# Kernel optimization log

Measured on AMD Instinct MI355X. Metric: run time of the kernel, lower is better.

## Reference

```python
import jax, jax.numpy as jnp
import numpy as np

K = 20          # args.k (minu=True)
EPS = 1e-5      # BatchNorm eps
BNS = float(1.0 / np.sqrt(1.0 + EPS))  # eval-mode BN with running_mean=0, running_var=1


def knn_idx(x, k):
    # x: (B, C, N); returns indices of k nearest neighbors (incl. self): (B, N, k)
    xx = jnp.sum(x * x, axis=1)                       # (B, N)
    inner = jnp.einsum('bcn,bcm->bnm', x, x)          # (B, N, N)
    dist = 2.0 * inner - xx[:, :, None] - xx[:, None, :]  # = -||xi - xj||^2
    return jax.lax.top_k(dist, k)[1]


def graph_feature(x, k):
    # x: (B, C, N) -> edge features (B, 2C, N, k) = cat(neighbor - center, center)
    idx = knn_idx(x, k)                               # (B, N, k)
    xt = jnp.transpose(x, (0, 2, 1))                  # (B, N, C)
    feat = jnp.take_along_axis(xt[:, None, :, :], idx[..., None], axis=2)  # (B, N, k, C)
    center = xt[:, :, None, :]
    out = jnp.concatenate([feat - center, jnp.broadcast_to(center, feat.shape)], axis=-1)
    return jnp.transpose(out, (0, 3, 1, 2))


def edge_block(x, w, g, b, k):
    # EdgeConv: gather -> 1x1 conv -> BN(eval) -> LeakyReLU(0.2) -> max over neighbors
    h = graph_feature(x, k)                           # (B, 2C, N, k)
    y = jnp.einsum('bcnk,oc->bonk', h, w)
    y = g[None, :, None, None] * (y * BNS) + b[None, :, None, None]
    y = jax.nn.leaky_relu(y, 0.2)
    return jnp.max(y, axis=-1)                        # (B, O, N)


def _bn1(v, g, b):
    return g * (v * BNS) + b


def setup_inputs() -> dict:
    key = jax.random.key(0)
    ks = jax.random.split(key, 32)
    B, C, N = 16, 6, 1024

    def w(k_, shape):
        return jax.random.normal(k_, shape, jnp.float32) / np.sqrt(shape[1])

    def gm(k_, n):
        return 1.0 + 0.1 * jax.random.normal(k_, (n,), jnp.float32)

    def bt(k_, n):
        return 0.1 * jax.random.normal(k_, (n,), jnp.float32)

    return {
        'x': jax.random.normal(ks[0], (B, C, N), jnp.float32),
        'disc': jax.random.normal(ks[1], (B, 1), jnp.float32),
        'w1': w(ks[2], (64, 12)),   'g1': gm(ks[3], 64),   'b1': bt(ks[4], 64),
        'w2': w(ks[5], (64, 128)),  'g2': gm(ks[6], 64),   'b2': bt(ks[7], 64),
        'w3': w(ks[8], (128, 128)), 'g3': gm(ks[9], 128),  'b3': bt(ks[10], 128),
        'w4': w(ks[11], (256, 256)),'g4': gm(ks[12], 256), 'b4': bt(ks[13], 256),
        'w5': w(ks[14], (1024, 512)),'g5': gm(ks[15], 1024),'b5': bt(ks[16], 1024),
        'wl1': w(ks[17], (256, 2048)),'g6': gm(ks[18], 256),'b6': bt(ks[19], 256),
        'wl2': w(ks[20], (128, 256)),'g7': gm(ks[21], 128),'b7': bt(ks[22], 128),
        'wl21': w(ks[23], (64, 128)),
        'wl22': w(ks[24], (32, 64)),'g8': gm(ks[25], 32), 'b8': bt(ks[26], 32),
        'wl3': w(ks[27], (90, 32)),
    }


def reference(x, disc, w1, g1, b1, w2, g2, b2, w3, g3, b3, w4, g4, b4,
              w5, g5, b5, wl1, g6, b6, wl2, g7, b7, wl21, wl22, g8, b8, wl3):
    # disc is accepted by the original forward but unused
    x1 = edge_block(x, w1, g1, b1, K)                 # (B, 64, N)
    x2 = edge_block(x1, w2, g2, b2, K)                # (B, 64, N)
    x3 = edge_block(x2, w3, g3, b3, K)                # (B, 128, N)
    x4 = edge_block(x3, w4, g4, b4, K)                # (B, 256, N)
    h = jnp.concatenate([x1, x2, x3, x4], axis=1)     # (B, 512, N)
    y = jnp.einsum('bcn,oc->bon', h, w5)              # conv5 1x1
    y = g5[None, :, None] * (y * BNS) + b5[None, :, None]
    y = jax.nn.leaky_relu(y, 0.2)                     # (B, emb, N)
    p = jnp.concatenate([jnp.max(y, axis=2), jnp.mean(y, axis=2)], axis=1)  # (B, 2*emb)
    z = jax.nn.leaky_relu(_bn1(p @ wl1.T, g6, b6), 0.2)
    z = jax.nn.leaky_relu(_bn1(z @ wl2.T, g7, b7), 0.2)
    z = jax.nn.gelu(_bn1((z @ wl21.T) @ wl22.T, g8, b8), approximate=False)
    return z @ wl3.T                                  # (B, 90)
```

## Files before the change

### kernel.cpp

```cpp
#include <hip/hip_runtime.h>
#include <math.h>
#include <float.h>

#define BNS_C 0.9999950000374996f

typedef __bf16 bf8 __attribute__((ext_vector_type(8)));
typedef float f4 __attribute__((ext_vector_type(4)));
union I4BF8 { int4 i; bf8 b; };

static __device__ __forceinline__ unsigned short f2bf(float f) {
    unsigned u = __float_as_uint(f);
    u += 0x7fff + ((u >> 16) & 1);
    return (unsigned short)(u >> 16);
}

__global__ void k_xin_t(const float* __restrict__ x, float* __restrict__ X0, float* __restrict__ xx) {
    int i = blockIdx.x * 256 + threadIdx.x;
    int b = i >> 10, n = i & 1023;
    const float* xb = x + (((size_t)b * 6) << 10) + n;
    float4* o4 = (float4*)(X0 + ((size_t)i << 3));
    float v0 = xb[0], v1 = xb[1 << 10], v2 = xb[2 << 10];
    float v3 = xb[3 << 10], v4 = xb[4 << 10], v5 = xb[5 << 10];
    o4[0] = make_float4(v0, v1, v2, v3);
    o4[1] = make_float4(v4, v5, 0.f, 0.f);
    xx[i] = v0*v0 + v1*v1 + v2*v2 + v3*v3 + v4*v4 + v5*v5;
}

__global__ __launch_bounds__(256) void k_gram2(const float* __restrict__ X, const float* __restrict__ xx,
                                               float* __restrict__ D, int Cp, int b0) {
    int z = blockIdx.z, b = b0 + z;
    int n0 = blockIdx.y * 64, m0 = blockIdx.x * 64;
    __shared__ float As[32 * 68], Bs[32 * 68];
    int tid = threadIdx.x;
    int ti = tid & 15, tj = tid >> 4;
    float acc[4][4] = {};
    const float* Xb = X + (((size_t)b) << 10) * Cp;
    for (int c0 = 0; c0 < Cp; c0 += 32) {
        for (int e = tid; e < 2048; e += 256) {
            int row = e >> 5, cc = e & 31, c = c0 + cc;
            float a = 0.f, bb = 0.f;
            if (c < Cp) {
                a  = Xb[(size_t)(n0 + row) * Cp + c];
                bb = Xb[(size_t)(m0 + row) * Cp + c];
            }
            As[cc * 68 + row] = a; Bs[cc * 68 + row] = bb;
        }
        __syncthreads();
#pragma unroll 8
        for (int cc = 0; cc < 32; ++cc) {
            const float4 av = *(const float4*)(As + cc * 68 + 4 * tj);
            const float4 bv = *(const float4*)(Bs + cc * 68 + 4 * ti);
            acc[0][0] += av.x * bv.x; acc[0][1] += av.x * bv.y; acc[0][2] += av.x * bv.z; acc[0][3] += av.x * bv.w;
            acc[1][0] += av.y * bv.x; acc[1][1] += av.y * bv.y; acc[1][2] += av.y * bv.z; acc[1][3] += av.y * bv.w;
            acc[2][0] += av.z * bv.x; acc[2][1] += av.z * bv.y; acc[2][2] += av.z * bv.z; acc[2][3] += av.z * bv.w;
            acc[3][0] += av.w * bv.x; acc[3][1] += av.w * bv.y; acc[3][2] += av.w * bv.z; acc[3][3] += av.w * bv.w;
        }
        __syncthreads();
    }
    const float4 xm = *(const float4*)(xx + (b << 10) + m0 + 4 * ti);
#pragma unroll
    for (int a = 0; a < 4; ++a) {
        int n = n0 + 4 * tj + a;
        float xn = xx[(b << 10) + n];
        float4 o;
        o.x = 2.f * acc[a][0] - xn - xm.x;
        o.y = 2.f * acc[a][1] - xn - xm.y;
        o.z = 2.f * acc[a][2] - xn - xm.z;
        o.w = 2.f * acc[a][3] - xn - xm.w;
        *(float4*)(D + ((size_t)((z << 10) + n) << 10) + m0 + 4 * ti) = o;
    }
}

#define CE(I,J) { if (kk[I] < kk[J]) { unsigned long long t_ = kk[I]; kk[I] = kk[J]; kk[J] = t_; } }
__global__ __launch_bounds__(256) void k_topk(const float* __restrict__ D, int* __restrict__ idxo, int b0) {
    __shared__ unsigned long long H[4096];
    int lane = threadIdx.x & 63, wv = threadIdx.x >> 6;
    int rl = blockIdx.x * 4 + wv;
    const float* row = D + ((size_t)rl << 10);
    unsigned long long kk[16];
#pragma unroll
    for (int j = 0; j < 16; ++j) {
        float v = row[lane + 64 * j];
        unsigned u = __float_as_uint(v);
        unsigned s = u ^ ((unsigned)(((int)u) >> 31) | 0x80000000u);
        int m = lane + (j << 6);
        kk[j] = ((unsigned long long)s << 32) | (unsigned)(1023 - m);
    }
    CE(0,1) CE(2,3) CE(0,2) CE(1,3) CE(1,2)
    CE(4,5) CE(6,7) CE(4,6) CE(5,7) CE(5,6)
    CE(0,4) CE(2,6) CE(2,4) CE(1,5) CE(3,7) CE(3,5) CE(1,2) CE(3,4) CE(5,6)
    CE(8,9) CE(10,11) CE(8,10) CE(9,11) CE(9,10)
    CE(12,13) CE(14,15) CE(12,14) CE(13,15) CE(13,14)
    CE(8,12) CE(10,14) CE(10,12) CE(9,13) CE(11,15) CE(11,13) CE(9,10) CE(11,12) CE(13,14)
    CE(0,8) CE(4,12) CE(4,8) CE(2,10) CE(6,14) CE(6,10) CE(2,4) CE(6,8) CE(10,12)
    CE(1,9) CE(5,13) CE(5,9) CE(3,11) CE(7,15) CE(7,11) CE(3,5) CE(7,9) CE(11,13)
    CE(1,2) CE(3,4) CE(5,6) CE(7,8) CE(9,10) CE(11,12) CE(13,14)
    unsigned long long* Hw = H + (wv << 10);
#pragma unroll
    for (int j = 0; j < 16; ++j) Hw[(j << 6) + lane] = kk[j];
    int ptr = 0;
    unsigned long long h = kk[0];
    int* outp = idxo + (size_t)((b0 << 10) + rl) * 20;
    for (int it = 0; it < 20; ++it) {
        unsigned long long bk = h;
#pragma unroll
        for (int off = 32; off; off >>= 1) {
            unsigned long long ok = __shfl_down(bk, off);
            if (ok > bk) bk = ok;
        }
        unsigned wlo = __builtin_amdgcn_readfirstlane((unsigned)bk);
        unsigned whi = __builtin_amdgcn_readfirstlane((unsigned)(bk >> 32));
        unsigned long long win = ((unsigned long long)whi << 32) | wlo;
        if (lane == 0) outp[it] = 1023 - (int)(wlo & 1023);
        if (h == win) {
            ++ptr;
            h = (ptr < 16) ? Hw[(ptr << 6) + lane] : 0ULL;
        }
    }
}
#undef CE

__global__ __launch_bounds__(256) void k_uv(const float* __restrict__ X, const float* __restrict__ w,
                                            float* __restrict__ V, float* __restrict__ U,
                                            int Cp, int C, int O) {
    int n0 = blockIdx.x * 64, o0 = blockIdx.y * 64, b = blockIdx.z;
    __shared__ float Xs[32 * 68], Was[32 * 68], Wds[32 * 68];
    int tid = threadIdx.x, ti = tid & 15, tj = tid >> 4;
    float accv[4][4] = {}, accu[4][4] = {};
    const float* Xb = X + (((size_t)b) << 10) * Cp;
    int W2 = 2 * C;
    for (int c0 = 0; c0 < Cp; c0 += 32) {
        for (int e = tid; e < 2048; e += 256) {
            int row = e >> 5, cc = e & 31, c = c0 + cc;
            Xs[cc * 68 + row] = (c < Cp) ? Xb[(size_t)(n0 + row) * Cp + c] : 0.f;
            float wa = 0.f, wd = 0.f;
            if (c < C) {
                float a_ = w[(size_t)(o0 + row) * W2 + c];
                float b_ = w[(size_t)(o0 + row) * W2 + C + c];
                wa = a_; wd = b_ - a_;
            }
            Was[cc * 68 + row] = wa; Wds[cc * 68 + row] = wd;
        }
        __syncthreads();
#pragma unroll 8
        for (int cc = 0; cc < 32; ++cc) {
            const float4 xv = *(const float4*)(Xs  + cc * 68 + 4 * tj);
            const float4 av = *(const float4*)(Was + cc * 68 + 4 * ti);
            const float4 dv = *(const float4*)(Wds + cc * 68 + 4 * ti);
            accv[0][0] += xv.x * av.x; accv[0][1] += xv.x * av.y; accv[0][2] += xv.x * av.z; accv[0][3] += xv.x * av.w;
            accv[1][0] += xv.y * av.x; accv[1][1] += xv.y * av.y; accv[1][2] += xv.y * av.z; accv[1][3] += xv.y * av.w;
            accv[2][0] += xv.z * av.x; accv[2][1] += xv.z * av.y; accv[2][2] += xv.z * av.z; accv[2][3] += xv.z * av.w;
            accv[3][0] += xv.w * av.x; accv[3][1] += xv.w * av.y; accv[3][2] += xv.w * av.z; accv[3][3] += xv.w * av.w;
            accu[0][0] += xv.x * dv.x; accu[0][1] += xv.x * dv.y; accu[0][2] += xv.x * dv.z; accu[0][3] += xv.x * dv.w;
            accu[1][0] += xv.y * dv.x; accu[1][1] += xv.y * dv.y; accu[1][2] += xv.y * dv.z; accu[1][3] += xv.y * dv.w;
            accu[2][0] += xv.z * dv.x; accu[2][1] += xv.z * dv.y; accu[2][2] += xv.z * dv.z; accu[2][3] += xv.z * dv.w;
            accu[3][0] += xv.w * dv.x; accu[3][1] += xv.w * dv.y; accu[3][2] += xv.w * dv.z; accu[3][3] += xv.w * dv.w;
        }
        __syncthreads();
    }
#pragma unroll
    for (int a = 0; a < 4; ++a) {
        int n = n0 + 4 * tj + a;
        size_t base = ((size_t)((b << 10) + n)) * O + o0 + 4 * ti;
        *(float4*)(V + base) = make_float4(accv[a][0], accv[a][1], accv[a][2], accv[a][3]);
        *(float4*)(U + base) = make_float4(accu[a][0], accu[a][1], accu[a][2], accu[a][3]);
    }
}

__global__ __launch_bounds__(256) void k_gmax(const float* __restrict__ V, const float* __restrict__ U,
                                              const int* __restrict__ idx,
                                              const float* __restrict__ gg, const float* __restrict__ bb,
                                              float* __restrict__ Xo, float* __restrict__ xx,
                                              unsigned short* __restrict__ HB, int coff, int O) {
    __shared__ float sxx[4];
    int tid = threadIdx.x;
    int Tn = 256 / O;
    int j = tid / O, o = tid - j * O;
    int pt = blockIdx.x * Tn + j;
    int b = pt >> 10, n = pt & 1023;
    float uv = U[(size_t)pt * O + o];
    float gv = gg[o], bv = bb[o];
    const int* ip = idx + (size_t)pt * 20;
    float mx = -FLT_MAX;
    for (int k = 0; k < 20; ++k) {
        int m = ip[k] & 1023;
        float vv = V[(size_t)((b << 10) + m) * O + o];
        float y = gv * ((vv + uv) * BNS_C) + bv;
        y = y > 0.f ? y : 0.2f * y;
        mx = fmaxf(mx, y);
    }
    Xo[(size_t)pt * O + o] = mx;
    int c = coff + o;
    HB[(((size_t)(b * 16 + (c >> 5)) << 10) + n) * 32 + (c & 31)] = f2bf(mx);
    float s = mx * mx;
#pragma unroll
    for (int off = 32; off; off >>= 1) s += __shfl_down(s, off);
    int wid = tid >> 6, lane = tid & 63;
    if (lane == 0) sxx[wid] = s;
    __syncthreads();
    if (o == 0) {
        int Wpp = O >> 6;
        float t = 0.f;
        for (int w = 0; w < Wpp; ++w) t += sxx[j * Wpp + w];
        xx[pt] = t;
    }
}

__global__ __launch_bounds__(256) void k_final_mfma(const unsigned short* __restrict__ HB,
                                                    const float* __restrict__ w5,
                                                    const float* __restrict__ g5,
                                                    const float* __restrict__ b5,
                                                    float* __restrict__ pp) {
    int b = blockIdx.x;
    int nt = blockIdx.z;
    int wv = threadIdx.x >> 6, lane = threadIdx.x & 63;
    int r = lane & 15, q = lane >> 4;
    int o = blockIdx.y * 64 + wv * 16 + r;
    bf8 Bfr[16];
    const float* wrow = w5 + (size_t)o * 512 + q * 8;
#pragma unroll
    for (int s = 0; s < 16; ++s) {
        float4 f0 = *(const float4*)(wrow + s * 32);
        float4 f1 = *(const float4*)(wrow + s * 32 + 4);
        I4BF8 u_;
        u_.i.x = f2bf(f0.x) | ((unsigned)f2bf(f0.y) << 16);
        u_.i.y = f2bf(f0.z) | ((unsigned)f2bf(f0.w) << 16);
        u_.i.z = f2bf(f1.x) | ((unsigned)f2bf(f1.y) << 16);
        u_.i.w = f2bf(f1.z) | ((unsigned)f2bf(f1.w) << 16);
        Bfr[s] = u_.b;
    }
    float gb = g5[o] * BNS_C, bv = b5[o];
    float mx = -FLT_MAX, sm = 0.f;
    for (int g = 0; g < 4; ++g) {
        int row0 = (nt << 8) + (g << 6);
        f4 C0 = {0.f, 0.f, 0.f, 0.f}, C1 = C0, C2 = C0, C3 = C0;
#pragma unroll
        for (int s = 0; s < 16; ++s) {
            const unsigned short* slab = HB + (((size_t)(b * 16 + s) << 10) + row0) * 32 + q * 8;
            I4BF8 A0, A1, A2, A3;
            A0.i = *(const int4*)(slab + (size_t)( 0 + r) * 32);
            A1.i = *(const int4*)(slab + (size_t)(16 + r) * 32);
            A2.i = *(const int4*)(slab + (size_t)(32 + r) * 32);
            A3.i = *(const int4*)(slab + (size_t)(48 + r) * 32);
            C0 = __builtin_amdgcn_mfma_f32_16x16x32_bf16(A0.b, Bfr[s], C0, 0, 0, 0);
            C1 = __builtin_amdgcn_mfma_f32_16x16x32_bf16(A1.b, Bfr[s], C1, 0, 0, 0);
            C2 = __builtin_amdgcn_mfma_f32_16x16x32_bf16(A2.b, Bfr[s], C2, 0, 0, 0);
            C3 = __builtin_amdgcn_mfma_f32_16x16x32_bf16(A3.b, Bfr[s], C3, 0, 0, 0);
        }
#pragma unroll
        for (int e = 0; e < 4; ++e) {
            float y0 = gb * C0[e] + bv; y0 = y0 > 0.f ? y0 : 0.2f * y0; mx = fmaxf(mx, y0); sm += y0;
            float y1 = gb * C1[e] + bv; y1 = y1 > 0.f ? y1 : 0.2f * y1; mx = fmaxf(mx, y1); sm += y1;
            float y2 = gb * C2[e] + bv; y2 = y2 > 0.f ? y2 : 0.2f * y2; mx = fmaxf(mx, y2); sm += y2;
            float y3 = gb * C3[e] + bv; y3 = y3 > 0.f ? y3 : 0.2f * y3; mx = fmaxf(mx, y3); sm += y3;
        }
    }
    mx = fmaxf(mx, __shfl_down(mx, 32)); sm += __shfl_down(sm, 32);
    mx = fmaxf(mx, __shfl_down(mx, 16)); sm += __shfl_down(sm, 16);
    if (q == 0) {
        float* pb = pp + (size_t)(nt * 16 + b) * 2048;
        pb[o] = mx;
        pb[1024 + o] = sm;
    }
}

__global__ __launch_bounds__(256) void k_fc2p(const float* __restrict__ pp, const float* __restrict__ w,
                                              const float* __restrict__ gg, const float* __restrict__ bb,
                                              float* __restrict__ out, int O) {
    int gw = blockIdx.x * 4 + (threadIdx.x >> 6);
    int lane = threadIdx.x & 63;
    int r = gw / O, o = gw - r * O;
    const float* wr = w + (size_t)o * 2048;
    float s = 0.f;
    for (int c = lane; c < 2048; c += 64) {
        const float* q0 = pp + (size_t)r * 2048 + c;
        float v;
        if (c < 1024) {
            v = fmaxf(fmaxf(q0[0], q0[16 * 2048]), fmaxf(q0[32 * 2048], q0[48 * 2048]));
        } else {
            v = (q0[0] + q0[16 * 2048] + q0[32 * 2048] + q0[48 * 2048]) * (1.f / 1024.f);
        }
        s += v * wr[c];
    }
#pragma unroll
    for (int off = 32; off; off >>= 1) s += __shfl_down(s, off);
    if (lane == 0) {
        float y = gg[o] * (s * BNS_C) + bb[o];
        out[gw] = y > 0.f ? y : 0.2f * y;
    }
}

__global__ __launch_bounds__(256) void k_fc_tail(const float* __restrict__ z1,
                                                 const float* __restrict__ wl2, const float* __restrict__ g7, const float* __restrict__ b7,
                                                 const float* __restrict__ wl21,
                                                 const float* __restrict__ wl22, const float* __restrict__ g8, const float* __restrict__ b8,
                                                 const float* __restrict__ wl3,
                                                 float* __restrict__ out) {
    __shared__ float L1[128], L2[64], L3[32];
    int r = blockIdx.x;
    int tid = threadIdx.x, lane = tid & 63, wv = tid >> 6;
    const float* ir = z1 + r * 256;
    float a0 = ir[lane], a1 = ir[lane + 64], a2 = ir[lane + 128], a3 = ir[lane + 192];
    for (int ob = 0; ob < 32; ob += 2) {
        int o0 = wv * 32 + ob, o1 = o0 + 1;
        const float* w0 = wl2 + (size_t)o0 * 256;
        const float* w1 = wl2 + (size_t)o1 * 256;
        float s0 = a0 * w0[lane] + a1 * w0[lane + 64] + a2 * w0[lane + 128] + a3 * w0[lane + 192];
        float s1 = a0 * w1[lane] + a1 * w1[lane + 64] + a2 * w1[lane + 128] + a3 * w1[lane + 192];
#pragma unroll
        for (int off = 32; off; off >>= 1) { s0 += __shfl_down(s0, off); s1 += __shfl_down(s1, off); }
        if (lane == 0) {
            float y0 = g7[o0] * (s0 * BNS_C) + b7[o0]; L1[o0] = y0 > 0.f ? y0 : 0.2f * y0;
            float y1 = g7[o1] * (s1 * BNS_C) + b7[o1]; L1[o1] = y1 > 0.f ? y1 : 0.2f * y1;
        }
    }
    __syncthreads();
    float b0v = L1[lane], b1v = L1[lane + 64];
    for (int ob = 0; ob < 16; ob += 2) {
        int o0 = wv * 16 + ob, o1 = o0 + 1;
        const float* w0 = wl21 + (size_t)o0 * 128;
        const float* w1 = wl21 + (size_t)o1 * 128;
        float s0 = b0v * w0[lane] + b1v * w0[lane + 64];
        float s1 = b0v * w1[lane] + b1v * w1[lane + 64];
#pragma unroll
        for (int off = 32; off; off >>= 1) { s0 += __shfl_down(s0, off); s1 += __shfl_down(s1, off); }
        if (lane == 0) { L2[o0] = s0; L2[o1] = s1; }
    }
    __syncthreads();
    float c0v = L2[lane];
    for (int ob = 0; ob < 8; ob += 2) {
        int o0 = wv * 8 + ob, o1 = o0 + 1;
        float s0 = c0v * wl22[(size_t)o0 * 64 + lane];
        float s1 = c0v * wl22[(size_t)o1 * 64 + lane];
#pragma unroll
        for (int off = 32; off; off >>= 1) { s0 += __shfl_down(s0, off); s1 += __shfl_down(s1, off); }
        if (lane == 0) {
            float y0 = g8[o0] * (s0 * BNS_C) + b8[o0];
            L3[o0] = 0.5f * y0 * (1.f + erff(y0 * 0.70710678118654752f));
            float y1 = g8[o1] * (s1 * BNS_C) + b8[o1];
            L3[o1] = 0.5f * y1 * (1.f + erff(y1 * 0.70710678118654752f));
        }
    }
    __syncthreads();
    float d0v = (lane < 32) ? L3[lane] : 0.f;
    for (int o = wv; o < 90; o += 4) {
        float s = (lane < 32) ? d0v * wl3[(size_t)o * 32 + lane] : 0.f;
#pragma unroll
        for (int off = 32; off; off >>= 1) s += __shfl_down(s, off);
        if (lane == 0) out[r * 90 + o] = s;
    }
}

extern "C" void kernel_launch(void* const* d_in, const int* in_sizes, int n_in,
                              void* d_out, int out_size, void* d_ws, size_t ws_size,
                              hipStream_t stream) {
    typedef const float* fp;
    fp x  = (fp)d_in[0];
    fp w1 = (fp)d_in[2],  g1 = (fp)d_in[3],  b1 = (fp)d_in[4];
    fp w2 = (fp)d_in[5],  g2 = (fp)d_in[6],  b2 = (fp)d_in[7];
    fp w3 = (fp)d_in[8],  g3 = (fp)d_in[9],  b3 = (fp)d_in[10];
    fp w4 = (fp)d_in[11], g4 = (fp)d_in[12], b4 = (fp)d_in[13];
    fp w5 = (fp)d_in[14], g5 = (fp)d_in[15], b5 = (fp)d_in[16];
    fp wl1 = (fp)d_in[17], g6 = (fp)d_in[18], b6 = (fp)d_in[19];
    fp wl2 = (fp)d_in[20], g7 = (fp)d_in[21], b7 = (fp)d_in[22];
    fp wl21 = (fp)d_in[23], wl22 = (fp)d_in[24];
    fp g8 = (fp)d_in[25], b8 = (fp)d_in[26], wl3 = (fp)d_in[27];

    char* ws = (char*)d_ws;
    size_t off = 0;
    auto alloc = [&](size_t floats) { float* p_ = (float*)(ws + off); off += floats * 4; off = (off + 255) & ~(size_t)255; return p_; };
    float* X0  = alloc(131072);
    float* X1  = alloc(1048576);
    float* X2  = alloc(1048576);
    float* X3  = alloc(2097152);
    float* X4  = alloc(4194304);
    float* xx  = alloc(16384);
    int*   nbr = (int*)alloc(327680);
    unsigned short* HB = (unsigned short*)alloc(4194304);
    float* pp  = alloc(131072);
    float* z1  = alloc(4096);
    size_t poolAvail = (ws_size > off) ? (ws_size - off) / 4 : 0;
    int fullD = poolAvail >= 16777216;
    float* pool = alloc(fullD ? 16777216 : 8388608);

    float* D = pool;
    float* V = pool;
    float* U = pool + 4194304;

    k_xin_t<<<64, 256, 0, stream>>>(x, X0, xx);

    struct Blk { const float* Xin; int Cp, C, O, coff; const float *w, *g, *b; float* Xout; };
    Blk blks[4] = {
        {X0, 8,   6,   64,  0,   w1, g1, b1, X1},
        {X1, 64,  64,  64,  64,  w2, g2, b2, X2},
        {X2, 64,  64,  128, 128, w3, g3, b3, X3},
        {X3, 128, 128, 256, 256, w4, g4, b4, X4},
    };
    for (int i = 0; i < 4; ++i) {
        const Blk& B_ = blks[i];
        if (fullD) {
            k_gram2<<<dim3(16, 16, 16), 256, 0, stream>>>(B_.Xin, xx, D, B_.Cp, 0);
            k_topk<<<4096, 256, 0, stream>>>(D, nbr, 0);
        } else {
            for (int b0 = 0; b0 < 16; b0 += 8) {
                k_gram2<<<dim3(16, 16, 8), 256, 0, stream>>>(B_.Xin, xx, D, B_.Cp, b0);
                k_topk<<<2048, 256, 0, stream>>>(D, nbr, b0);
            }
        }
        k_uv<<<dim3(16, B_.O / 64, 16), 256, 0, stream>>>(B_.Xin, B_.w, V, U, B_.Cp, B_.C, B_.O);
        int Tn = 256 / B_.O;
        k_gmax<<<16384 / Tn, 256, 0, stream>>>(V, U, nbr, B_.g, B_.b, B_.Xout, xx, HB, B_.coff, B_.O);
    }

    k_final_mfma<<<dim3(16, 16, 4), 256, 0, stream>>>(HB, w5, g5, b5, pp);

    k_fc2p<<<(16 * 256) / 4, 256, 0, stream>>>(pp, wl1, g6, b6, z1, 256);
    k_fc_tail<<<16, 256, 0, stream>>>(z1, wl2, g7, b7, wl21, wl22, g8, b8, wl3, (float*)d_out);
}
```

Measured before the change: 837.4 us.

## Pipeline final MFMA loads, split points over more blocks, vectorize top-k row reads

The final conv5 MFMA kernel now splits the 1024 points into 8 tiles of 128 instead of 4 of 256. Inside each tile it keeps eight accumulators and a three-stage register ring that prefetches A fragments two channel slabs ahead, so load latency overlaps the MFMAs. It also sets a two-blocks-per-CU launch bound, doubles the partial-pool buffer, and updates the FC reducer to combine 8 partials. The top-k kernel reads each distance row with float4 loads instead of scalar strided loads; the index is encoded in each key, so the per-lane element order does not matter. The trade-offs are higher register pressure, which the launch bound may force into spills, and a little more partial-reduction traffic.

New measurement: 870.5 us. 1.04x slower.

```diff
diff --git a/kernel.cpp b/kernel.cpp
--- a/kernel.cpp
+++ b/kernel.cpp
@@ -79,12 +79,16 @@
     const float* row = D + ((size_t)rl << 10);
     unsigned long long kk[16];
 #pragma unroll
-    for (int j = 0; j < 16; ++j) {
-        float v = row[lane + 64 * j];
-        unsigned u = __float_as_uint(v);
-        unsigned s = u ^ ((unsigned)(((int)u) >> 31) | 0x80000000u);
-        int m = lane + (j << 6);
-        kk[j] = ((unsigned long long)s << 32) | (unsigned)(1023 - m);
+    for (int jj = 0; jj < 4; ++jj) {
+        const float4 v4 = *(const float4*)(row + (jj << 8) + (lane << 2));
+        const float vv[4] = {v4.x, v4.y, v4.z, v4.w};
+#pragma unroll
+        for (int e = 0; e < 4; ++e) {
+            unsigned u = __float_as_uint(vv[e]);
+            unsigned s = u ^ ((unsigned)(((int)u) >> 31) | 0x80000000u);
+            int m = (jj << 8) + (lane << 2) + e;
+            kk[jj * 4 + e] = ((unsigned long long)s << 32) | (unsigned)(1023 - m);
+        }
     }
     CE(0,1) CE(2,3) CE(0,2) CE(1,3) CE(1,2)
     CE(4,5) CE(6,7) CE(4,6) CE(5,7) CE(5,6)
@@ -206,11 +210,11 @@
     }
 }
 
-__global__ __launch_bounds__(256) void k_final_mfma(const unsigned short* __restrict__ HB,
-                                                    const float* __restrict__ w5,
-                                                    const float* __restrict__ g5,
-                                                    const float* __restrict__ b5,
-                                                    float* __restrict__ pp) {
+__global__ __launch_bounds__(256, 2) void k_final_mfma(const unsigned short* __restrict__ HB,
+                                                       const float* __restrict__ w5,
+                                                       const float* __restrict__ g5,
+                                                       const float* __restrict__ b5,
+                                                       float* __restrict__ pp) {
     int b = blockIdx.x;
     int nt = blockIdx.z;
     int wv = threadIdx.x >> 6, lane = threadIdx.x & 63;
@@ -230,31 +234,38 @@
         Bfr[s] = u_.b;
     }
     float gb = g5[o] * BNS_C, bv = b5[o];
+    int row0 = nt << 7;
+    f4 C[8];
+#pragma unroll
+    for (int c = 0; c < 8; ++c) C[c] = (f4){0.f, 0.f, 0.f, 0.f};
+    I4BF8 A[3][8];
+#pragma unroll
+    for (int st = 0; st < 2; ++st)
+#pragma unroll
+        for (int c = 0; c < 8; ++c)
+            A[st][c].i = *(const int4*)(HB + (((size_t)(b * 16 + st) << 10) + row0 + c * 16 + r) * 32 + q * 8);
+#pragma unroll
+    for (int s = 0; s < 16; ++s) {
+        if (s + 2 < 16) {
+            int st = (s + 2) % 3;
+#pragma unroll
+            for (int c = 0; c < 8; ++c)
+                A[st][c].i = *(const int4*)(HB + (((size_t)(b * 16 + s + 2) << 10) + row0 + c * 16 + r) * 32 + q * 8);
+        }
+        int cu = s % 3;
+#pragma unroll
+        for (int c = 0; c < 8; ++c)
+            C[c] = __builtin_amdgcn_mfma_f32_16x16x32_bf16(A[cu][c].b, Bfr[s], C[c], 0, 0, 0);
+    }
     float mx = -FLT_MAX, sm = 0.f;
-    for (int g = 0; g < 4; ++g) {
-        int row0 = (nt << 8) + (g << 6);
-        f4 C0 = {0.f, 0.f, 0.f, 0.f}, C1 = C0, C2 = C0, C3 = C0;
-#pragma unroll
-        for (int s = 0; s < 16; ++s) {
-            const unsigned short* slab = HB + (((size_t)(b * 16 + s) << 10) + row0) * 32 + q * 8;
-            I4BF8 A0, A1, A2, A3;
-            A0.i = *(const int4*)(slab + (size_t)( 0 + r) * 32);
-            A1.i = *(const int4*)(slab + (size_t)(16 + r) * 32);
-            A2.i = *(const int4*)(slab + (size_t)(32 + r) * 32);
-            A3.i = *(const int4*)(slab + (size_t)(48 + r) * 32);
-            C0 = __builtin_amdgcn_mfma_f32_16x16x32_bf16(A0.b, Bfr[s], C0, 0, 0, 0);
-            C1 = __builtin_amdgcn_mfma_f32_16x16x32_bf16(A1.b, Bfr[s], C1, 0, 0, 0);
-            C2 = __builtin_amdgcn_mfma_f32_16x16x32_bf16(A2.b, Bfr[s], C2, 0, 0, 0);
-            C3 = __builtin_amdgcn_mfma_f32_16x16x32_bf16(A3.b, Bfr[s], C3, 0, 0, 0);
-        }
+#pragma unroll
+    for (int c = 0; c < 8; ++c)
 #pragma unroll
         for (int e = 0; e < 4; ++e) {
-            float y0 = gb * C0[e] + bv; y0 = y0 > 0.f ? y0 : 0.2f * y0; mx = fmaxf(mx, y0); sm += y0;
-            float y1 = gb * C1[e] + bv; y1 = y1 > 0.f ? y1 : 0.2f * y1; mx = fmaxf(mx, y1); sm += y1;
-            float y2 = gb * C2[e] + bv; y2 = y2 > 0.f ? y2 : 0.2f * y2; mx = fmaxf(mx, y2); sm += y2;
-            float y3 = gb * C3[e] + bv; y3 = y3 > 0.f ? y3 : 0.2f * y3; mx = fmaxf(mx, y3); sm += y3;
-        }
-    }
+            float y = gb * C[c][e] + bv;
+            y = y > 0.f ? y : 0.2f * y;
+            mx = fmaxf(mx, y); sm += y;
+        }
     mx = fmaxf(mx, __shfl_down(mx, 32)); sm += __shfl_down(sm, 32);
     mx = fmaxf(mx, __shfl_down(mx, 16)); sm += __shfl_down(sm, 16);
     if (q == 0) {
@@ -276,9 +287,15 @@
         const float* q0 = pp + (size_t)r * 2048 + c;
         float v;
         if (c < 1024) {
-            v = fmaxf(fmaxf(q0[0], q0[16 * 2048]), fmaxf(q0[32 * 2048], q0[48 * 2048]));
+            float m0 = fmaxf(q0[0 * 32768], q0[1 * 32768]);
+            float m1 = fmaxf(q0[2 * 32768], q0[3 * 32768]);
+            float m2 = fmaxf(q0[4 * 32768], q0[5 * 32768]);
+            float m3 = fmaxf(q0[6 * 32768], q0[7 * 32768]);
+            v = fmaxf(fmaxf(m0, m1), fmaxf(m2, m3));
         } else {
-            v = (q0[0] + q0[16 * 2048] + q0[32 * 2048] + q0[48 * 2048]) * (1.f / 1024.f);
+            float s0 = q0[0 * 32768] + q0[1 * 32768] + q0[2 * 32768] + q0[3 * 32768];
+            float s1 = q0[4 * 32768] + q0[5 * 32768] + q0[6 * 32768] + q0[7 * 32768];
+            v = (s0 + s1) * (1.f / 1024.f);
         }
         s += v * wr[c];
     }
@@ -377,7 +394,7 @@
     float* xx  = alloc(16384);
     int*   nbr = (int*)alloc(327680);
     unsigned short* HB = (unsigned short*)alloc(4194304);
-    float* pp  = alloc(131072);
+    float* pp  = alloc(262144);
     float* z1  = alloc(4096);
     size_t poolAvail = (ws_size > off) ? (ws_size - off) / 4 : 0;
     int fullD = poolAvail >= 16777216;
@@ -412,7 +429,7 @@
         k_gmax<<<16384 / Tn, 256, 0, stream>>>(V, U, nbr, B_.g, B_.b, B_.Xout, xx, HB, B_.coff, B_.O);
     }
 
-    k_final_mfma<<<dim3(16, 16, 4), 256, 0, stream>>>(HB, w5, g5, b5, pp);
+    k_final_mfma<<<dim3(16, 16, 8), 256, 0, stream>>>(HB, w5, g5, b5, pp);
 
     k_fc2p<<<(16 * 256) / 4, 256, 0, stream>>>(pp, wl1, g6, b6, z1, 256);
     k_fc_tail<<<16, 256, 0, stream>>>(z1, wl2, g7, b7, wl21, wl22, g8, b8, wl3, (float*)d_out);
```
